# Performance work log

Hardware: AMD Instinct MI355X
Metric: run time of the kernel (lower is better)

## Reference

```python
import jax, jax.numpy as jnp
import numpy as np

B, T, N, C = 2, 12, 4096, 32
FILTERS = [32, 32, 32]


def setup_inputs() -> dict:
    key = jax.random.key(0)
    ks = jax.random.split(key, 12)
    inp = {
        'data': jax.random.normal(ks[0], (B, T, N, C), dtype=jnp.float32),
        'adj': jax.random.uniform(ks[1], (3 * N, 3 * N), dtype=jnp.float32) / (3.0 * N),
        'temporal_emb': jax.random.normal(ks[2], (1, T, 1, C), dtype=jnp.float32) * 0.0003,
        'spatial_emb': jax.random.normal(ks[3], (1, 1, N, C), dtype=jnp.float32) * 0.0003,
    }
    c_in = C
    for i, f in enumerate(FILTERS):
        scale = 1.0 / np.sqrt(c_in)
        inp[f'W{i}'] = jax.random.uniform(ks[4 + 2 * i], (c_in, 2 * f), dtype=jnp.float32,
                                          minval=-scale, maxval=scale)
        inp[f'b{i}'] = jnp.zeros((2 * f,), dtype=jnp.float32)
        c_in = f
    return inp


def reference(data, adj, temporal_emb, spatial_emb, W0, b0, W1, b1, W2, b2):
    # data: (B, T, N, C). Add temporal + spatial position embeddings.
    x = data + temporal_emb + spatial_emb
    b, t, n, c = x.shape
    w = t - 2  # number of sliding windows
    # Gather all 3-step windows at once: (B, W, 3, N, C) -> (B, W, 3N, C)
    idx = jnp.arange(w)[:, None] + jnp.arange(3)[None, :]
    xw = x[:, idx].reshape(b, w, 3 * n, c)
    outs = []
    for Wl, bl in ((W0, b0), (W1, b1), (W2, b2)):
        # dense graph conv over the 3N local graph, batched over (B, W)
        xw = jnp.einsum('nm,bwmc->bwnc', adj, xw)
        y = xw @ Wl + bl            # (B, W, 3N, 2*C')
        lhs, rhs = jnp.split(y, 2, axis=-1)
        xw = lhs * jax.nn.sigmoid(rhs)  # GLU, (B, W, 3N, C')
        outs.append(xw[:, :, n:2 * n, :])  # crop middle timestep
    # stacked max over the gcn layers: (B, T-2, N, C_last)
    return jnp.max(jnp.stack(outs, axis=0), axis=0)
```

## Files before the change

### kernel.cpp

```cpp
#include <hip/hip_runtime.h>

#define NN 4096
#define TT 12
#define CC 32
#define WW 10
#define K3 12288
#define NCOL 640
#define SA 4096.0f
#define SX 1024.0f
#define BM 96
#define BNH 320
#define BK 32
#define NT (K3 / BK)
#define ASTEP (768L * 512L)
#define BSTEP (40L * 512L)

typedef _Float16 half8 __attribute__((ext_vector_type(8)));
typedef float floatx4 __attribute__((ext_vector_type(4)));


__global__ __launch_bounds__(256) void k_conv_adj(const float* __restrict__ adj,
                                                  _Float16* __restrict__ a16) {
    __shared__ _Float16 tile[16][520];
    int m16 = blockIdx.x;
    int kc  = blockIdx.y;
    long m0 = (long)m16 * 16;
    long k0 = (long)kc * 512;
    int t = threadIdx.x;
    const float4* src = (const float4*)adj;
#pragma unroll
    for (int rep = 0; rep < 8; ++rep) {
        int idx = rep * 256 + t;
        int row = idx >> 7, c4 = idx & 127;
        float4 v = src[((m0 + row) * K3 + k0) / 4 + c4];
        tile[row][c4 * 4 + 0] = (_Float16)(v.x * SA);
        tile[row][c4 * 4 + 1] = (_Float16)(v.y * SA);
        tile[row][c4 * 4 + 2] = (_Float16)(v.z * SA);
        tile[row][c4 * 4 + 3] = (_Float16)(v.w * SA);
    }
    __syncthreads();
#pragma unroll
    for (int rep = 0; rep < 4; ++rep) {
        int slot = rep * 256 + t;
        int kt = slot >> 6, l = slot & 63;
        half8 h;
#pragma unroll
        for (int j = 0; j < 8; ++j)
            h[j] = tile[l & 15][kt * 32 + (l >> 4) * 8 + j];
        *(half8*)(a16 + ((long)(kc * 16 + kt) * 768 + m16) * 512 + l * 8) = h;
    }
}

__global__ void k_prep(const float* __restrict__ data, const float* __restrict__ temb,
                       const float* __restrict__ semb, _Float16* __restrict__ x0t) {
    __shared__ float sb[CC][64 + 1];
    int z = blockIdx.y;
    int b = z / 30; int r = z % 30; int w = r / 3; int j3 = r % 3;
    int t = w + j3;
    int n0 = blockIdx.x * 64;
    int tid = threadIdx.x;
    for (int e = tid; e < 64 * CC; e += 256) {
        int nl = e >> 5, c = e & 31;
        float v = data[((long)(b * TT + t) * NN + n0 + nl) * CC + c]
                + temb[t * CC + c] + semb[(n0 + nl) * CC + c];
        sb[c][nl] = v;
    }
    __syncthreads();
    int bw = b * WW + w;
    int w4 = tid >> 6, l = tid & 63;
    int ct = w4 >> 1, kt = w4 & 1;
    int c = ct * 16 + (l & 15);
    int kb = kt * 32 + (l >> 4) * 8;
    half8 h;
#pragma unroll
    for (int j = 0; j < 8; ++j) h[j] = (_Float16)sb[c][kb + j];
    long k32 = (long)j3 * 128 + (n0 >> 5) + kt;
    *(half8*)(x0t + (k32 * 40 + bw * 2 + ct) * 512 + l * 8) = h;
}

template <int MODE>
__global__ __launch_bounds__(512, 1) void k_gemm_glu(
    const _Float16* __restrict__ A, const _Float16* __restrict__ BT,
    const float* __restrict__ Wt, const float* __restrict__ bias,
    _Float16* __restrict__ outH,
    const _Float16* __restrict__ x1, const _Float16* __restrict__ x2,
    float* __restrict__ outF,
    float invS, int mBase, int Mvalid)
{
    __shared__ float scr[BM * 321];
    __shared__ float WB[CC * 64 + 64];
    const int SCRW = 321;

    int tid = threadIdx.x;
    int lane = tid & 63, wid = tid >> 6;
    int wm = wid >> 2, wn = wid & 3;

    int nblk = gridDim.x;
    int q = nblk >> 3, r = nblk & 7;
    int xcd = blockIdx.x & 7, bi = blockIdx.x >> 3;
    int lin = (xcd < r ? xcd * (q + 1) : r * (q + 1) + (xcd - r) * q) + bi;
    int mt = lin >> 1, nh = lin & 1;
    long m0 = (long)mt * BM;
    int n0 = nh * BNH;

    for (int e = tid; e < CC * 64; e += 512) WB[e] = Wt[e];
    if (tid < 64) WB[CC * 64 + tid] = bias[tid];

    int m16b = (int)((mBase + m0) >> 4) + wm * 3;
    const _Float16* aP0 = A + (long)(m16b + 0) * 512 + lane * 8;
    const _Float16* aP1 = A + (long)(m16b + 1) * 512 + lane * 8;
    const _Float16* aP2 = A + (long)(m16b + 2) * 512 + lane * 8;
    int c16 = (n0 >> 4) + wn * 5;
    const _Float16* bP0 = BT + (long)(c16 + 0) * 512 + lane * 8;
    const _Float16* bP1 = BT + (long)(c16 + 1) * 512 + lane * 8;
    const _Float16* bP2 = BT + (long)(c16 + 2) * 512 + lane * 8;
    const _Float16* bP3 = BT + (long)(c16 + 3) * 512 + lane * 8;
    const _Float16* bP4 = BT + (long)(c16 + 4) * 512 + lane * 8;

    floatx4 acc[3][5] = {};

#define LOAD_SET(sa0, sa1, sa2, sb0, sb1, sb2, sb3, sb4, OA, OB)   \
    do {                                                           \
        sa0 = *(const half8*)(aP0 + (OA));                         \
        sa1 = *(const half8*)(aP1 + (OA));                         \
        sa2 = *(const half8*)(aP2 + (OA));                         \
        sb0 = *(const half8*)(bP0 + (OB));                         \
        sb1 = *(const half8*)(bP1 + (OB));                         \
        sb2 = *(const half8*)(bP2 + (OB));                         \
        sb3 = *(const half8*)(bP3 + (OB));                         \
        sb4 = *(const half8*)(bP4 + (OB));                         \
    } while (0)

#define MFMA_SET(sa0, sa1, sa2, sb0, sb1, sb2, sb3, sb4)                              \
    do {                                                                              \
        acc[0][0] = __builtin_amdgcn_mfma_f32_16x16x32_f16(sa0, sb0, acc[0][0],0,0,0);\
        acc[0][1] = __builtin_amdgcn_mfma_f32_16x16x32_f16(sa0, sb1, acc[0][1],0,0,0);\
        acc[0][2] = __builtin_amdgcn_mfma_f32_16x16x32_f16(sa0, sb2, acc[0][2],0,0,0);\
        acc[0][3] = __builtin_amdgcn_mfma_f32_16x16x32_f16(sa0, sb3, acc[0][3],0,0,0);\
        acc[0][4] = __builtin_amdgcn_mfma_f32_16x16x32_f16(sa0, sb4, acc[0][4],0,0,0);\
        acc[1][0] = __builtin_amdgcn_mfma_f32_16x16x32_f16(sa1, sb0, acc[1][0],0,0,0);\
        acc[1][1] = __builtin_amdgcn_mfma_f32_16x16x32_f16(sa1, sb1, acc[1][1],0,0,0);\
        acc[1][2] = __builtin_amdgcn_mfma_f32_16x16x32_f16(sa1, sb2, acc[1][2],0,0,0);\
        acc[1][3] = __builtin_amdgcn_mfma_f32_16x16x32_f16(sa1, sb3, acc[1][3],0,0,0);\
        acc[1][4] = __builtin_amdgcn_mfma_f32_16x16x32_f16(sa1, sb4, acc[1][4],0,0,0);\
        acc[2][0] = __builtin_amdgcn_mfma_f32_16x16x32_f16(sa2, sb0, acc[2][0],0,0,0);\
        acc[2][1] = __builtin_amdgcn_mfma_f32_16x16x32_f16(sa2, sb1, acc[2][1],0,0,0);\
        acc[2][2] = __builtin_amdgcn_mfma_f32_16x16x32_f16(sa2, sb2, acc[2][2],0,0,0);\
        acc[2][3] = __builtin_amdgcn_mfma_f32_16x16x32_f16(sa2, sb3, acc[2][3],0,0,0);\
        acc[2][4] = __builtin_amdgcn_mfma_f32_16x16x32_f16(sa2, sb4, acc[2][4],0,0,0);\
    } while (0)

    half8 aA0, aA1, aA2, bA0, bA1, bA2, bA3, bA4;
    half8 aB0, aB1, aB2, bB0, bB1, bB2, bB3, bB4;

    LOAD_SET(aA0, aA1, aA2, bA0, bA1, bA2, bA3, bA4, 0, 0);
    LOAD_SET(aB0, aB1, aB2, bB0, bB1, bB2, bB3, bB4, ASTEP, BSTEP);
    aP0 += 2 * ASTEP; aP1 += 2 * ASTEP; aP2 += 2 * ASTEP;
    bP0 += 2 * BSTEP; bP1 += 2 * BSTEP; bP2 += 2 * BSTEP; bP3 += 2 * BSTEP; bP4 += 2 * BSTEP;

#pragma unroll 1
    for (int t = 0; t + 3 < NT; t += 2) {
        MFMA_SET(aA0, aA1, aA2, bA0, bA1, bA2, bA3, bA4);
        LOAD_SET(aA0, aA1, aA2, bA0, bA1, bA2, bA3, bA4, 0, 0);
        MFMA_SET(aB0, aB1, aB2, bB0, bB1, bB2, bB3, bB4);
        LOAD_SET(aB0, aB1, aB2, bB0, bB1, bB2, bB3, bB4, ASTEP, BSTEP);
        aP0 += 2 * ASTEP; aP1 += 2 * ASTEP; aP2 += 2 * ASTEP;
        bP0 += 2 * BSTEP; bP1 += 2 * BSTEP; bP2 += 2 * BSTEP; bP3 += 2 * BSTEP; bP4 += 2 * BSTEP;
    }
    MFMA_SET(aA0, aA1, aA2, bA0, bA1, bA2, bA3, bA4);
    MFMA_SET(aB0, aB1, aB2, bB0, bB1, bB2, bB3, bB4);
#undef LOAD_SET
#undef MFMA_SET

    int rb = (lane >> 4) * 4, cb = lane & 15;

    __syncthreads();
#pragma unroll
    for (int ms = 0; ms < 3; ++ms)
#pragma unroll
        for (int ns = 0; ns < 5; ++ns)
#pragma unroll
            for (int i = 0; i < 4; ++i)
                scr[(wm * 48 + ms * 16 + rb + i) * SCRW + wn * 80 + ns * 16 + cb] = acc[ms][ns][i];
    __syncthreads();

    for (int e = tid; e < BM * 10; e += 512) {
        int row = e % BM;
        int bwl = e / BM;
        int bw = nh * 10 + bwl;
        long m = m0 + row;
        float g[CC];
#pragma unroll
        for (int c = 0; c < CC; ++c) g[c] = scr[row * SCRW + bwl * 32 + c] * invS;
        float y[64];
#pragma unroll
        for (int o = 0; o < 64; ++o) y[o] = WB[CC * 64 + o];
#pragma unroll
        for (int c = 0; c < CC; ++c) {
            float gv = g[c];
#pragma unroll
            for (int o = 0; o < 64; ++o) y[o] = fmaf(gv, WB[c * 64 + o], y[o]);
        }
        if (MODE == 0) {
            long k32 = m >> 5;
            int kb16 = ((int)(m >> 3) & 3) * 16;
            int kj = (int)(m & 7);
#pragma unroll
            for (int c = 0; c < CC; ++c) {
                float rr = y[c] * (1.f / (1.f + __expf(-y[c + 32])));
                long dst = ((k32 * 40) + (bw * 2 + (c >> 4))) * 512
                         + ((c & 15) + kb16) * 8 + kj;
                outH[dst] = (_Float16)(rr * SX);
            }
        } else {
            if (m < Mvalid) {
                long kk = NN + m;
                long k32 = kk >> 5;
                int kb16 = ((int)(kk >> 3) & 3) * 16;
                int kj = (int)(kk & 7);
                float res[CC];
#pragma unroll
                for (int c = 0; c < CC; ++c) {
                    float rr = y[c] * (1.f / (1.f + __expf(-y[c + 32])));
                    long idx = ((k32 * 40) + (bw * 2 + (c >> 4))) * 512
                             + ((c & 15) + kb16) * 8 + kj;
                    float v1 = (float)x1[idx] * (1.f / SX);
                    float v2 = (float)x2[idx] * (1.f / SX);
                    res[c] = fmaxf(rr, fmaxf(v1, v2));
                }
                float4* op = (float4*)(outF + ((long)bw * NN + m) * CC);
#pragma unroll
                for (int qv = 0; qv < CC / 4; ++qv)
                    op[qv] = make_float4(res[qv * 4 + 0], res[qv * 4 + 1],
                                         res[qv * 4 + 2], res[qv * 4 + 3]);
            }
        }
    }
}

extern "C" void kernel_launch(void* const* d_in, const int* in_sizes, int n_in,
                              void* d_out, int out_size, void* d_ws, size_t ws_size,
                              hipStream_t stream)
{
    const float* data = (const float*)d_in[0];
    const float* adj  = (const float*)d_in[1];
    const float* temb = (const float*)d_in[2];
    const float* semb = (const float*)d_in[3];
    const float* W0 = (const float*)d_in[4];
    const float* b0 = (const float*)d_in[5];
    const float* W1 = (const float*)d_in[6];
    const float* b1 = (const float*)d_in[7];
    const float* W2 = (const float*)d_in[8];
    const float* b2 = (const float*)d_in[9];
    float* out = (float*)d_out;
    (void)ws_size; (void)in_sizes; (void)n_in; (void)out_size;

    char* ws = (char*)d_ws;
    _Float16* A16 = (_Float16*)ws;  ws += (size_t)K3 * K3 * 2;
    _Float16* X0  = (_Float16*)ws;  ws += (size_t)NCOL * K3 * 2;
    _Float16* X1  = (_Float16*)ws;  ws += (size_t)NCOL * K3 * 2;
    _Float16* X2  = (_Float16*)ws;  ws += (size_t)NCOL * K3 * 2;

    k_conv_adj<<<dim3(768, 24), 256, 0, stream>>>(adj, A16);
    k_prep<<<dim3(64, 60), 256, 0, stream>>>(data, temb, semb, X0);

    k_gemm_glu<0><<<256, 512, 0, stream>>>(A16, X0, W0, b0, X1,
                                           nullptr, nullptr, nullptr, 1.f / SA, 0, K3);
    k_gemm_glu<0><<<256, 512, 0, stream>>>(A16, X1, W1, b1, X2,
                                           nullptr, nullptr, nullptr, 1.f / (SA * SX), 0, K3);
    k_gemm_glu<1><<<86, 512, 0, stream>>>(A16, X2, W2, b2, nullptr,
                                          X1, X2, out, 1.f / (SA * SX), NN, NN);
}
```

Measured before the change: 1.281 ms.

## Deepen GEMM register prefetch to three stages with MFMA priority and nontemporal B loads

Moves the main adjacency GEMM loop from double to triple register buffering, so loads for three K-tiles are in flight while MFMAs run. It also raises wave priority around each MFMA burst with s_setprio and marks the B operand loads nontemporal to reduce cache pollution. NT (384) is divisible by 3, so the loop count and tail stay consistent. The extra buffer set adds 64 VGPRs per thread, which may lower occupancy or cause spills at 512 threads per block.

Result: slower. 4.964 ms (+287.4%).

```diff
diff --git a/kernel.cpp b/kernel.cpp
--- a/kernel.cpp
+++ b/kernel.cpp
@@ -119,58 +119,74 @@
 
     floatx4 acc[3][5] = {};
 
-#define LOAD_SET(sa0, sa1, sa2, sb0, sb1, sb2, sb3, sb4, OA, OB)   \
-    do {                                                           \
-        sa0 = *(const half8*)(aP0 + (OA));                         \
-        sa1 = *(const half8*)(aP1 + (OA));                         \
-        sa2 = *(const half8*)(aP2 + (OA));                         \
-        sb0 = *(const half8*)(bP0 + (OB));                         \
-        sb1 = *(const half8*)(bP1 + (OB));                         \
-        sb2 = *(const half8*)(bP2 + (OB));                         \
-        sb3 = *(const half8*)(bP3 + (OB));                         \
-        sb4 = *(const half8*)(bP4 + (OB));                         \
+#define DECL_SET(S) half8 a0##S, a1##S, a2##S, b0##S, b1##S, b2##S, b3##S, b4##S;
+
+#define LOAD_SET(S, T)                                                         \
+    do {                                                                       \
+        a0##S = *(const half8*)(aP0 + (T) * ASTEP);                            \
+        a1##S = *(const half8*)(aP1 + (T) * ASTEP);                            \
+        a2##S = *(const half8*)(aP2 + (T) * ASTEP);                            \
+        b0##S = __builtin_nontemporal_load((const half8*)(bP0 + (T) * BSTEP)); \
+        b1##S = __builtin_nontemporal_load((const half8*)(bP1 + (T) * BSTEP)); \
+        b2##S = __builtin_nontemporal_load((const half8*)(bP2 + (T) * BSTEP)); \
+        b3##S = __builtin_nontemporal_load((const half8*)(bP3 + (T) * BSTEP)); \
+        b4##S = __builtin_nontemporal_load((const half8*)(bP4 + (T) * BSTEP)); \
     } while (0)
 
-#define MFMA_SET(sa0, sa1, sa2, sb0, sb1, sb2, sb3, sb4)                              \
-    do {                                                                              \
-        acc[0][0] = __builtin_amdgcn_mfma_f32_16x16x32_f16(sa0, sb0, acc[0][0],0,0,0);\
-        acc[0][1] = __builtin_amdgcn_mfma_f32_16x16x32_f16(sa0, sb1, acc[0][1],0,0,0);\
-        acc[0][2] = __builtin_amdgcn_mfma_f32_16x16x32_f16(sa0, sb2, acc[0][2],0,0,0);\
-        acc[0][3] = __builtin_amdgcn_mfma_f32_16x16x32_f16(sa0, sb3, acc[0][3],0,0,0);\
-        acc[0][4] = __builtin_amdgcn_mfma_f32_16x16x32_f16(sa0, sb4, acc[0][4],0,0,0);\
-        acc[1][0] = __builtin_amdgcn_mfma_f32_16x16x32_f16(sa1, sb0, acc[1][0],0,0,0);\
-        acc[1][1] = __builtin_amdgcn_mfma_f32_16x16x32_f16(sa1, sb1, acc[1][1],0,0,0);\
-        acc[1][2] = __builtin_amdgcn_mfma_f32_16x16x32_f16(sa1, sb2, acc[1][2],0,0,0);\
-        acc[1][3] = __builtin_amdgcn_mfma_f32_16x16x32_f16(sa1, sb3, acc[1][3],0,0,0);\
-        acc[1][4] = __builtin_amdgcn_mfma_f32_16x16x32_f16(sa1, sb4, acc[1][4],0,0,0);\
-        acc[2][0] = __builtin_amdgcn_mfma_f32_16x16x32_f16(sa2, sb0, acc[2][0],0,0,0);\
-        acc[2][1] = __builtin_amdgcn_mfma_f32_16x16x32_f16(sa2, sb1, acc[2][1],0,0,0);\
-        acc[2][2] = __builtin_amdgcn_mfma_f32_16x16x32_f16(sa2, sb2, acc[2][2],0,0,0);\
-        acc[2][3] = __builtin_amdgcn_mfma_f32_16x16x32_f16(sa2, sb3, acc[2][3],0,0,0);\
-        acc[2][4] = __builtin_amdgcn_mfma_f32_16x16x32_f16(sa2, sb4, acc[2][4],0,0,0);\
+#define MFMA_SET(S)                                                                       \
+    do {                                                                                  \
+        __builtin_amdgcn_s_setprio(1);                                                    \
+        acc[0][0] = __builtin_amdgcn_mfma_f32_16x16x32_f16(a0##S, b0##S, acc[0][0],0,0,0);\
+        acc[0][1] = __builtin_amdgcn_mfma_f32_16x16x32_f16(a0##S, b1##S, acc[0][1],0,0,0);\
+        acc[0][2] = __builtin_amdgcn_mfma_f32_16x16x32_f16(a0##S, b2##S, acc[0][2],0,0,0);\
+        acc[0][3] = __builtin_amdgcn_mfma_f32_16x16x32_f16(a0##S, b3##S, acc[0][3],0,0,0);\
+        acc[0][4] = __builtin_amdgcn_mfma_f32_16x16x32_f16(a0##S, b4##S, acc[0][4],0,0,0);\
+        acc[1][0] = __builtin_amdgcn_mfma_f32_16x16x32_f16(a1##S, b0##S, acc[1][0],0,0,0);\
+        acc[1][1] = __builtin_amdgcn_mfma_f32_16x16x32_f16(a1##S, b1##S, acc[1][1],0,0,0);\
+        acc[1][2] = __builtin_amdgcn_mfma_f32_16x16x32_f16(a1##S, b2##S, acc[1][2],0,0,0);\
+        acc[1][3] = __builtin_amdgcn_mfma_f32_16x16x32_f16(a1##S, b3##S, acc[1][3],0,0,0);\
+        acc[1][4] = __builtin_amdgcn_mfma_f32_16x16x32_f16(a1##S, b4##S, acc[1][4],0,0,0);\
+        acc[2][0] = __builtin_amdgcn_mfma_f32_16x16x32_f16(a2##S, b0##S, acc[2][0],0,0,0);\
+        acc[2][1] = __builtin_amdgcn_mfma_f32_16x16x32_f16(a2##S, b1##S, acc[2][1],0,0,0);\
+        acc[2][2] = __builtin_amdgcn_mfma_f32_16x16x32_f16(a2##S, b2##S, acc[2][2],0,0,0);\
+        acc[2][3] = __builtin_amdgcn_mfma_f32_16x16x32_f16(a2##S, b3##S, acc[2][3],0,0,0);\
+        acc[2][4] = __builtin_amdgcn_mfma_f32_16x16x32_f16(a2##S, b4##S, acc[2][4],0,0,0);\
+        __builtin_amdgcn_s_setprio(0);                                                    \
     } while (0)
 
-    half8 aA0, aA1, aA2, bA0, bA1, bA2, bA3, bA4;
-    half8 aB0, aB1, aB2, bB0, bB1, bB2, bB3, bB4;
-
-    LOAD_SET(aA0, aA1, aA2, bA0, bA1, bA2, bA3, bA4, 0, 0);
-    LOAD_SET(aB0, aB1, aB2, bB0, bB1, bB2, bB3, bB4, ASTEP, BSTEP);
-    aP0 += 2 * ASTEP; aP1 += 2 * ASTEP; aP2 += 2 * ASTEP;
-    bP0 += 2 * BSTEP; bP1 += 2 * BSTEP; bP2 += 2 * BSTEP; bP3 += 2 * BSTEP; bP4 += 2 * BSTEP;
+#define ADV3()                                                    \
+    do {                                                          \
+        aP0 += 3 * ASTEP; aP1 += 3 * ASTEP; aP2 += 3 * ASTEP;     \
+        bP0 += 3 * BSTEP; bP1 += 3 * BSTEP; bP2 += 3 * BSTEP;     \
+        bP3 += 3 * BSTEP; bP4 += 3 * BSTEP;                       \
+    } while (0)
+
+    DECL_SET(X)
+    DECL_SET(Y)
+    DECL_SET(Z)
+
+    LOAD_SET(X, 0);
+    LOAD_SET(Y, 1);
+    LOAD_SET(Z, 2);
+    ADV3();
 
 #pragma unroll 1
-    for (int t = 0; t + 3 < NT; t += 2) {
-        MFMA_SET(aA0, aA1, aA2, bA0, bA1, bA2, bA3, bA4);
-        LOAD_SET(aA0, aA1, aA2, bA0, bA1, bA2, bA3, bA4, 0, 0);
-        MFMA_SET(aB0, aB1, aB2, bB0, bB1, bB2, bB3, bB4);
-        LOAD_SET(aB0, aB1, aB2, bB0, bB1, bB2, bB3, bB4, ASTEP, BSTEP);
-        aP0 += 2 * ASTEP; aP1 += 2 * ASTEP; aP2 += 2 * ASTEP;
-        bP0 += 2 * BSTEP; bP1 += 2 * BSTEP; bP2 += 2 * BSTEP; bP3 += 2 * BSTEP; bP4 += 2 * BSTEP;
-    }
-    MFMA_SET(aA0, aA1, aA2, bA0, bA1, bA2, bA3, bA4);
-    MFMA_SET(aB0, aB1, aB2, bB0, bB1, bB2, bB3, bB4);
+    for (int t = 0; t + 5 < NT; t += 3) {
+        MFMA_SET(X);
+        LOAD_SET(X, 0);
+        MFMA_SET(Y);
+        LOAD_SET(Y, 1);
+        MFMA_SET(Z);
+        LOAD_SET(Z, 2);
+        ADV3();
+    }
+    MFMA_SET(X);
+    MFMA_SET(Y);
+    MFMA_SET(Z);
+#undef DECL_SET
 #undef LOAD_SET
 #undef MFMA_SET
+#undef ADV3
 
     int rb = (lane >> 4) * 4, cb = lane & 15;
 
```
